# Kernel optimization log

Measured on AMD Instinct MI355X. Metric: run time of the kernel, lower is better.

The kernel has to match this reference:

```python
import jax, jax.numpy as jnp
import numpy as np

N = 50000
E = 800000
IN_C, HID_C, OUT_C = 512, 256, 64
K = 10
ALPHA = 0.1


def setup_inputs() -> dict:
    key = jax.random.key(0)
    k1, k2, k3, k4, k5, k6 = jax.random.split(key, 6)
    x = jax.random.normal(k1, (N, IN_C), dtype=jnp.float32)
    edge_index = jax.random.randint(k2, (2, E), 0, N, dtype=jnp.int64)
    # Linear params (torch nn.Linear: y = x @ W.T + b), kaiming-ish scale
    W1 = jax.random.normal(k3, (HID_C, IN_C), dtype=jnp.float32) / np.sqrt(IN_C)
    b1 = jax.random.normal(k4, (HID_C,), dtype=jnp.float32) * 0.01
    W2 = jax.random.normal(k5, (OUT_C, HID_C), dtype=jnp.float32) / np.sqrt(HID_C)
    b2 = jax.random.normal(k6, (OUT_C,), dtype=jnp.float32) * 0.01
    return {"x": x, "edge_index": edge_index, "W1": W1, "b1": b1, "W2": W2, "b2": b2}


def reference(x, edge_index, W1, b1, W2, b2):
    # MLP head (dropout is identity in eval mode)
    h = jax.nn.relu(x @ W1.T + b1)          # [N, HID_C]
    z = h @ W2.T + b2                        # [N, OUT_C]

    src = edge_index[0]                      # message source
    dst = edge_index[1]                      # message target (aggregation index)

    # GCN symmetric normalization with self-loops (PyG APPNP default)
    ones = jnp.ones((E,), dtype=z.dtype)
    deg = jax.ops.segment_sum(ones, dst, num_segments=N) + 1.0  # +1 for self-loop
    dinv = jax.lax.rsqrt(deg)                # deg^{-1/2}
    edge_norm = (dinv[src] * dinv[dst])[:, None]   # [E, 1]
    self_norm = (dinv * dinv)[:, None]             # [N, 1] self-loop weight

    def step(hcur, _):
        agg = jax.ops.segment_sum(hcur[src] * edge_norm, dst, num_segments=N)
        agg = agg + hcur * self_norm
        hnew = (1.0 - ALPHA) * agg + ALPHA * z
        return hnew, None

    h_final, _ = jax.lax.scan(step, z, None, length=K)
    return h_final
```

## Files before the change

kernel.cpp:

```cpp
#include <hip/hip_runtime.h>

typedef __bf16 bf16x8 __attribute__((ext_vector_type(8)));
typedef float f32x4 __attribute__((ext_vector_type(4)));
typedef short short8 __attribute__((ext_vector_type(8)));

__device__ __forceinline__ unsigned short f2bf_u(float f) {
    unsigned u = __builtin_bit_cast(unsigned, f);
    u += 0x7FFFu + ((u >> 16) & 1u);
    return (unsigned short)(u >> 16);
}
__device__ __forceinline__ float bf2f(unsigned short h) {
    unsigned u = ((unsigned)h) << 16;
    return __builtin_bit_cast(float, u);
}
__device__ __forceinline__ float i2f(int b) { return __builtin_bit_cast(float, b); }

#define GLOAD_LDS16(gsrc, ldst)                                                        \
    __builtin_amdgcn_global_load_lds((const __attribute__((address_space(1))) void*)(gsrc), \
                                     (__attribute__((address_space(3))) void*)(ldst), 16, 0, 0)

__global__ __launch_bounds__(256)
void prep_a(const void* __restrict__ ei, const float* __restrict__ W1,
            const float* __restrict__ W2, int* __restrict__ flag,
            short* __restrict__ W1h, short* __restrict__ W1l,
            short* __restrict__ W2h, short* __restrict__ W2l) {
    const int tid = threadIdx.x;
    const int gtid = blockIdx.x * 256 + tid;
    const int gsize = gridDim.x * 256;
    if (blockIdx.x == 0) {
        unsigned v = 0;
        for (int i = tid * 2 + 1; i < 2048; i += 512) v |= ((const unsigned*)ei)[i];
        if (v) atomicOr(flag, 1);
    }
    const int n1 = 256 * 512, n2 = 64 * 256;
    for (int i = gtid; i < n1; i += gsize) {
        float w0 = W1[i];
        unsigned short h = f2bf_u(w0);
        W1h[i] = (short)h;
        W1l[i] = (short)f2bf_u(w0 - bf2f(h));
    }
    for (int i = gtid; i < n2; i += gsize) {
        float w0 = W2[i];
        unsigned short h = f2bf_u(w0);
        W2h[i] = (short)h;
        W2l[i] = (short)f2bf_u(w0 - bf2f(h));
    }
}

__global__ void convert_count_kernel(const void* __restrict__ edges, const int* __restrict__ flag,
                                     int* __restrict__ src, int* __restrict__ dst,
                                     int* __restrict__ counts, int E) {
    int e = blockIdx.x * 256 + threadIdx.x;
    if (e >= E) return;
    int s, d;
    if (*flag) { const int* p = (const int*)edges; s = p[e]; d = p[E + e]; }
    else       { const long long* p = (const long long*)edges; s = (int)p[e]; d = (int)p[E + e]; }
    src[e] = s;
    dst[e] = d;
    atomicAdd(&counts[d], 1);
}

__global__ void bsum_dinv_kernel(const int* __restrict__ counts, float* __restrict__ dinv,
                                 int* __restrict__ bs, int n) {
    __shared__ int sdata[256];
    int i = blockIdx.x * 256 + threadIdx.x;
    int v = (i < n) ? counts[i] : 0;
    if (i < n) dinv[i] = rsqrtf((float)v + 1.0f);
    sdata[threadIdx.x] = v;
    __syncthreads();
    #pragma unroll
    for (int off = 128; off > 0; off >>= 1) {
        if (threadIdx.x < off) sdata[threadIdx.x] += sdata[threadIdx.x + off];
        __syncthreads();
    }
    if (threadIdx.x == 0) bs[blockIdx.x] = sdata[0];
}

__global__ void scanbs_kernel(const int* __restrict__ bs, int* __restrict__ bsoff, int nb) {
    __shared__ int sdata[256];
    int tid = threadIdx.x;
    int v = (tid < nb) ? bs[tid] : 0;
    sdata[tid] = v;
    __syncthreads();
    #pragma unroll
    for (int off = 1; off < 256; off <<= 1) {
        int t = (tid >= off) ? sdata[tid - off] : 0;
        __syncthreads();
        sdata[tid] += t;
        __syncthreads();
    }
    if (tid < nb) bsoff[tid] = sdata[tid] - v;
}

__global__ void scanblock_kernel(const int* __restrict__ counts, const int* __restrict__ bsoff,
                                 int* __restrict__ rowptr, int* __restrict__ cursor, int n) {
    __shared__ int sdata[256];
    int tid = threadIdx.x;
    int i = blockIdx.x * 256 + tid;
    int v = (i < n) ? counts[i] : 0;
    sdata[tid] = v;
    __syncthreads();
    #pragma unroll
    for (int off = 1; off < 256; off <<= 1) {
        int t = (tid >= off) ? sdata[tid - off] : 0;
        __syncthreads();
        sdata[tid] += t;
        __syncthreads();
    }
    int excl = bsoff[blockIdx.x] + sdata[tid] - v;
    if (i < n) { rowptr[i] = excl; cursor[i] = excl; }
    if (i == n - 1) rowptr[n] = excl + v;
}

__global__ void fill_kernel(const int* __restrict__ src, const int* __restrict__ dst,
                            const float* __restrict__ dinv, int* __restrict__ cursor,
                            int2* __restrict__ csr, int E) {
    int e = blockIdx.x * 256 + threadIdx.x;
    if (e >= E) return;
    int s = src[e], d = dst[e];
    int pos = atomicAdd(&cursor[d], 1);
    float w = dinv[s] * dinv[d];
    csr[pos] = make_int2(s, __builtin_bit_cast(int, w));
}

__global__ __launch_bounds__(512)
void gemm1f_k(const float* __restrict__ x, const short* __restrict__ Bh,
              const short* __restrict__ Bl, const float* __restrict__ bias,
              short* __restrict__ C, int M) {
    extern __shared__ short lds[];
    short* sA  = lds;
    short* sBh = lds + 16384;
    short* sBl = lds + 49152;
    const int KDIM = 512, LDC = 256;
    const int tid = threadIdx.x, lane = tid & 63, wave = tid >> 6;
    const int wr = wave >> 2, wc = wave & 3;
    const int m0 = blockIdx.x * 128;
    const int lr = lane & 15, lk = lane >> 4;
    const int l8r = lane >> 3, l8u = lane & 7;
    const int tr = tid >> 3, tk = tid & 7;

    f32x4 acc[4][4];
    #pragma unroll
    for (int mi = 0; mi < 4; ++mi)
        #pragma unroll
        for (int ni = 0; ni < 4; ++ni) acc[mi][ni] = {0.f, 0.f, 0.f, 0.f};

    float4 fa[2][2];

    auto a_load = [&](int k0) {
        #pragma unroll
        for (int p = 0; p < 2; ++p) {
            int row = p * 64 + tr;
            int grow = m0 + row; if (grow > M - 1) grow = M - 1;
            const float* s = x + (size_t)grow * KDIM + k0 + tk * 8;
            fa[p][0] = *reinterpret_cast<const float4*>(s);
            fa[p][1] = *reinterpret_cast<const float4*>(s + 4);
        }
    };
    auto a_write = [&](int buf) {
        #pragma unroll
        for (int p = 0; p < 2; ++p) {
            int row = p * 64 + tr;
            short8 sh;
            sh[0] = (short)f2bf_u(fa[p][0].x); sh[1] = (short)f2bf_u(fa[p][0].y);
            sh[2] = (short)f2bf_u(fa[p][0].z); sh[3] = (short)f2bf_u(fa[p][0].w);
            sh[4] = (short)f2bf_u(fa[p][1].x); sh[5] = (short)f2bf_u(fa[p][1].y);
            sh[6] = (short)f2bf_u(fa[p][1].z); sh[7] = (short)f2bf_u(fa[p][1].w);
            *reinterpret_cast<short8*>(&sA[buf * 8192 + row * 64 + ((tk ^ (row & 7)) << 3)]) = sh;
        }
    };
    auto b_dma = [&](int buf, int k0) {
        #pragma unroll
        for (int p = 0; p < 4; ++p) {
            int row = p * 64 + wave * 8 + l8r;
            size_t goff = (size_t)row * KDIM + k0 + ((l8u ^ (row & 7)) << 3);
            GLOAD_LDS16(Bh + goff, sBh + buf * 16384 + (p * 64 + wave * 8) * 64);
            GLOAD_LDS16(Bl + goff, sBl + buf * 16384 + (p * 64 + wave * 8) * 64);
        }
    };

    a_load(0);
    b_dma(0, 0);
    asm volatile("s_waitcnt vmcnt(0)" ::: "memory");
    a_write(0);
    __syncthreads();

    int cur = 0;
    #pragma unroll 1
    for (int t = 0; t < 8; ++t) {
        const bool pf = (t < 7);
        if (pf) {
            a_load((t + 1) * 64);
            b_dma(cur ^ 1, (t + 1) * 64);
        }
        #pragma unroll
        for (int ks = 0; ks < 2; ++ks) {
            int kg = ks * 4 + lk;
            bf16x8 af[4], bhf[4], blf[4];
            #pragma unroll
            for (int mi = 0; mi < 4; ++mi) {
                int row = wr * 64 + mi * 16 + lr;
                af[mi] = *reinterpret_cast<const bf16x8*>(
                    &sA[cur * 8192 + row * 64 + ((kg ^ (row & 7)) << 3)]);
            }
            #pragma unroll
            for (int ni = 0; ni < 4; ++ni) {
                int row = wc * 64 + ni * 16 + lr;
                int idx = cur * 16384 + row * 64 + ((kg ^ (row & 7)) << 3);
                bhf[ni] = *reinterpret_cast<const bf16x8*>(&sBh[idx]);
                blf[ni] = *reinterpret_cast<const bf16x8*>(&sBl[idx]);
            }
            #pragma unroll
            for (int mi = 0; mi < 4; ++mi)
                #pragma unroll
                for (int ni = 0; ni < 4; ++ni) {
                    acc[mi][ni] = __builtin_amdgcn_mfma_f32_16x16x32_bf16(af[mi], bhf[ni], acc[mi][ni], 0, 0, 0);
                    acc[mi][ni] = __builtin_amdgcn_mfma_f32_16x16x32_bf16(af[mi], blf[ni], acc[mi][ni], 0, 0, 0);
                }
        }
        asm volatile("s_waitcnt vmcnt(0)" ::: "memory");
        if (pf) a_write(cur ^ 1);
        __syncthreads();
        cur ^= 1;
    }

    #pragma unroll
    for (int ni = 0; ni < 4; ++ni) {
        int col = wc * 64 + ni * 16 + lr;
        float bv = bias[col];
        #pragma unroll
        for (int mi = 0; mi < 4; ++mi) {
            #pragma unroll
            for (int r = 0; r < 4; ++r) {
                int row = m0 + wr * 64 + mi * 16 + lk * 4 + r;
                if (row < M) {
                    float v = fmaxf(acc[mi][ni][r] + bv, 0.0f);
                    C[(size_t)row * LDC + col] = (short)f2bf_u(v);
                }
            }
        }
    }
}

template<int KDIM, int LDC, bool AF32, bool RELU>
__device__ __forceinline__
void gemm_tile(const void* __restrict__ Av, const short* __restrict__ Bh,
               const short* __restrict__ Bl, const float* __restrict__ bias,
               short* __restrict__ C, int M, int m0, int n0,
               short* sAp, short* sBp) {
    constexpr int NT = KDIM / 64;
    const int tid  = threadIdx.x;
    const int lane = tid & 63;
    const int wave = tid >> 6;
    const int wr = wave >> 1, wc = wave & 1;
    const int lr = lane & 15;
    const int lk = lane >> 4;
    const int l8r = lane >> 3;
    const int l8u = lane & 7;
    const int tr = tid >> 3;
    const int tk = tid & 7;

    f32x4 acc[2][2];
    #pragma unroll
    for (int mi = 0; mi < 2; ++mi)
        #pragma unroll
        for (int ni = 0; ni < 2; ++ni) acc[mi][ni] = {0.f, 0.f, 0.f, 0.f};

    float4 fa[2][2];

    auto a_load = [&](int k0) {
        #pragma unroll
        for (int p = 0; p < 2; ++p) {
            int row = p * 64 + tr;
            int grow = m0 + row; if (grow > M - 1) grow = M - 1;
            const float* s = (const float*)Av + (size_t)grow * KDIM + k0 + tk * 8;
            fa[p][0] = *reinterpret_cast<const float4*>(s);
            fa[p][1] = *reinterpret_cast<const float4*>(s + 4);
        }
    };
    auto a_write = [&](int buf) {
        #pragma unroll
        for (int p = 0; p < 2; ++p) {
            int row = p * 64 + tr;
            short8 sh;
            sh[0] = (short)f2bf_u(fa[p][0].x); sh[1] = (short)f2bf_u(fa[p][0].y);
            sh[2] = (short)f2bf_u(fa[p][0].z); sh[3] = (short)f2bf_u(fa[p][0].w);
            sh[4] = (short)f2bf_u(fa[p][1].x); sh[5] = (short)f2bf_u(fa[p][1].y);
            sh[6] = (short)f2bf_u(fa[p][1].z); sh[7] = (short)f2bf_u(fa[p][1].w);
            *reinterpret_cast<short8*>(&sAp[buf * 8192 + row * 64 + ((tk ^ (row & 7)) << 3)]) = sh;
        }
    };
    auto a_dma = [&](int buf, int k0) {
        #pragma unroll
        for (int p = 0; p < 2; ++p) {
            int row = p * 64 + wave * 8 + l8r;
            int grow = m0 + row; if (grow > M - 1) grow = M - 1;
            const short* s = (const short*)Av + (size_t)grow * KDIM + k0 + ((l8u ^ (row & 7)) << 3);
            GLOAD_LDS16(s, sAp + buf * 8192 + p * 4096 + wave * 512);
        }
    };
    auto b_dma = [&](int buf, int k0) {
        int row = wave * 8 + l8r;
        size_t goff = (size_t)(n0 + row) * KDIM + k0 + ((l8u ^ (row & 7)) << 3);
        GLOAD_LDS16(Bh + goff, sBp + (buf * 2 + 0) * 4096 + wave * 512);
        GLOAD_LDS16(Bl + goff, sBp + (buf * 2 + 1) * 4096 + wave * 512);
    };

    if (AF32) {
        a_load(0);
        b_dma(0, 0);
        asm volatile("s_waitcnt vmcnt(0)" ::: "memory");
        a_write(0);
        __syncthreads();
    } else {
        a_dma(0, 0);
        b_dma(0, 0);
        asm volatile("s_waitcnt vmcnt(0)" ::: "memory");
        __builtin_amdgcn_s_barrier();
        asm volatile("" ::: "memory");
    }

    int cur = 0;
    #pragma unroll 1
    for (int t = 0; t < NT; ++t) {
        const bool pf = (t + 1 < NT);
        if (pf) {
            if (AF32) a_load((t + 1) * 64);
            else      a_dma(cur ^ 1, (t + 1) * 64);
            b_dma(cur ^ 1, (t + 1) * 64);
        }
        #pragma unroll
        for (int ks = 0; ks < 2; ++ks) {
            int kg = ks * 4 + lk;
            bf16x8 af[2], bhf[2], blf[2];
            #pragma unroll
            for (int mi = 0; mi < 2; ++mi) {
                int row = wr * 32 + mi * 16 + lr;
                af[mi] = *reinterpret_cast<const bf16x8*>(
                    &sAp[cur * 8192 + row * 64 + ((kg ^ (row & 7)) << 3)]);
            }
            #pragma unroll
            for (int ni = 0; ni < 2; ++ni) {
                int row = wc * 32 + ni * 16 + lr;
                int idx = row * 64 + ((kg ^ (row & 7)) << 3);
                bhf[ni] = *reinterpret_cast<const bf16x8*>(&sBp[(cur * 2 + 0) * 4096 + idx]);
                blf[ni] = *reinterpret_cast<const bf16x8*>(&sBp[(cur * 2 + 1) * 4096 + idx]);
            }
            #pragma unroll
            for (int mi = 0; mi < 2; ++mi)
                #pragma unroll
                for (int ni = 0; ni < 2; ++ni) {
                    acc[mi][ni] = __builtin_amdgcn_mfma_f32_16x16x32_bf16(af[mi], bhf[ni], acc[mi][ni], 0, 0, 0);
                    acc[mi][ni] = __builtin_amdgcn_mfma_f32_16x16x32_bf16(af[mi], blf[ni], acc[mi][ni], 0, 0, 0);
                }
        }
        asm volatile("s_waitcnt vmcnt(0)" ::: "memory");
        if (AF32) { if (pf) a_write(cur ^ 1); __syncthreads(); }
        else { __builtin_amdgcn_s_barrier(); asm volatile("" ::: "memory"); }
        cur ^= 1;
    }

    #pragma unroll
    for (int ni = 0; ni < 2; ++ni) {
        int col = n0 + wc * 32 + ni * 16 + lr;
        float bv = bias[col];
        #pragma unroll
        for (int mi = 0; mi < 2; ++mi) {
            #pragma unroll
            for (int r = 0; r < 4; ++r) {
                int row = m0 + wr * 32 + mi * 16 + lk * 4 + r;
                if (row < M) {
                    float v = acc[mi][ni][r] + bv;
                    if (RELU) v = fmaxf(v, 0.0f);
                    C[(size_t)row * LDC + col] = (short)f2bf_u(v);
                }
            }
        }
    }
}

__global__ __launch_bounds__(512)
void gemm1_k(const float* __restrict__ x, const short* __restrict__ W1h,
             const short* __restrict__ W1l, const float* __restrict__ b1,
             short* __restrict__ Hbf, int M) {
    __shared__ short sAp[2 * 128 * 64];
    __shared__ short sBp[2 * 2 * 64 * 64];
    int t = blockIdx.x;
    gemm_tile<512, 256, true, true>(x, W1h, W1l, b1, Hbf, M, (t >> 2) * 128, (t & 3) * 64, sAp, sBp);
}

__global__ __launch_bounds__(512)
void gemm2_k(const short* __restrict__ Hbf, const short* __restrict__ W2h,
             const short* __restrict__ W2l, const float* __restrict__ b2,
             short* __restrict__ zbf, int M) {
    __shared__ short sAp[2 * 128 * 64];
    __shared__ short sBp[2 * 2 * 64 * 64];
    gemm_tile<256, 64, false, false>(Hbf, W2h, W2l, b2, zbf, M, blockIdx.x * 128, 0, sAp, sBp);
}

__global__ __launch_bounds__(256)
void prop_step(const unsigned short* __restrict__ hin, const unsigned short* __restrict__ zbf,
               const int* __restrict__ rowptr, const int2* __restrict__ csr,
               const float* __restrict__ dinv, void* __restrict__ hout,
               int outf32, int n) {
    int node = blockIdx.x * 4 + (threadIdx.x >> 6);
    int lane = threadIdx.x & 63;
    if (node >= n) return;
    float di = dinv[node];
    int base = node << 6;
    float acc = bf2f(hin[base + lane]) * (di * di);
    int e = rowptr[node], e1 = rowptr[node + 1];

    if (e + 8 <= e1) {
        int2 r[8];
        #pragma unroll
        for (int j = 0; j < 8; ++j) r[j] = csr[e + j];
        for (; e + 16 <= e1; e += 8) {
            int2 rn[8];
            #pragma unroll
            for (int j = 0; j < 8; ++j) rn[j] = csr[e + 8 + j];
            unsigned short v[8];
            #pragma unroll
            for (int j = 0; j < 8; ++j) v[j] = hin[((unsigned)r[j].x << 6) + lane];
            #pragma unroll
            for (int j = 0; j < 8; ++j) acc = fmaf(bf2f(v[j]), i2f(r[j].y), acc);
            #pragma unroll
            for (int j = 0; j < 8; ++j) r[j] = rn[j];
        }
        {
            unsigned short v[8];
            #pragma unroll
            for (int j = 0; j < 8; ++j) v[j] = hin[((unsigned)r[j].x << 6) + lane];
            #pragma unroll
            for (int j = 0; j < 8; ++j) acc = fmaf(bf2f(v[j]), i2f(r[j].y), acc);
            e += 8;
        }
    }
    for (; e + 4 <= e1; e += 4) {
        int2 r[4]; unsigned short v[4];
        #pragma unroll
        for (int j = 0; j < 4; ++j) r[j] = csr[e + j];
        #pragma unroll
        for (int j = 0; j < 4; ++j) v[j] = hin[((unsigned)r[j].x << 6) + lane];
        #pragma unroll
        for (int j = 0; j < 4; ++j) acc = fmaf(bf2f(v[j]), i2f(r[j].y), acc);
    }
    for (; e < e1; ++e) {
        int2 r = csr[e];
        acc = fmaf(bf2f(hin[((unsigned)r.x << 6) + lane]), i2f(r.y), acc);
    }

    float res = 0.9f * acc + 0.1f * bf2f(zbf[base + lane]);
    if (outf32) ((float*)hout)[base + lane] = res;
    else        ((unsigned short*)hout)[base + lane] = f2bf_u(res);
}

extern "C" void kernel_launch(void* const* d_in, const int* in_sizes, int n_in,
                              void* d_out, int out_size, void* d_ws, size_t ws_size,
                              hipStream_t stream) {
    const float* x  = (const float*)d_in[0];
    const void*  ei = d_in[1];
    const float* W1 = (const float*)d_in[2];
    const float* b1 = (const float*)d_in[3];
    const float* W2 = (const float*)d_in[4];
    const float* b2 = (const float*)d_in[5];
    float* dout = (float*)d_out;

    const int IN_C = 512, HID_C = 256, OUT_C = 64, Ksteps = 10;
    const int N = in_sizes[0] / IN_C;
    const int E = in_sizes[1] / 2;

    char* w = (char*)d_ws;
    auto alloc = [&](size_t bytes) { char* p = w; w += (bytes + 255) & ~(size_t)255; return p; };
    int*   flag    = (int*)  alloc(4);
    int*   src32   = (int*)  alloc((size_t)E * 4);
    int*   dst32   = (int*)  alloc((size_t)E * 4);
    int*   counts  = (int*)  alloc((size_t)N * 4);
    int*   rowptr  = (int*)  alloc((size_t)(N + 1) * 4);
    int*   cursor  = (int*)  alloc((size_t)N * 4);
    float* dinv    = (float*)alloc((size_t)N * 4);
    int2*  csr     = (int2*) alloc((size_t)E * 8);
    short* W1h     = (short*)alloc((size_t)HID_C * IN_C * 2);
    short* W1l     = (short*)alloc((size_t)HID_C * IN_C * 2);
    short* W2h     = (short*)alloc((size_t)OUT_C * HID_C * 2);
    short* W2l     = (short*)alloc((size_t)OUT_C * HID_C * 2);
    short* Hbf     = (short*)alloc((size_t)N * HID_C * 2);
    unsigned short* zbf = (unsigned short*)alloc((size_t)N * OUT_C * 2);
    unsigned short* hA  = (unsigned short*)alloc((size_t)N * OUT_C * 2);
    unsigned short* hB  = (unsigned short*)alloc((size_t)N * OUT_C * 2);
    int*   bs      = (int*)  alloc(256 * 4);
    int*   bsoff   = (int*)  alloc(256 * 4);

    hipMemsetAsync(flag, 0, 4, stream);
    hipMemsetAsync(counts, 0, (size_t)N * 4, stream);

    const int egrid = (E + 255) / 256;
    const int nblk = (N + 255) / 256;
    const int mgrid = (N + 127) / 128;
    const int pgrid = (N + 3) / 4;

    prep_a<<<512, 256, 0, stream>>>(ei, W1, W2, flag, W1h, W1l, W2h, W2l);
    convert_count_kernel<<<egrid, 256, 0, stream>>>(ei, flag, src32, dst32, counts, E);
    bsum_dinv_kernel<<<nblk, 256, 0, stream>>>(counts, dinv, bs, N);
    scanbs_kernel<<<1, 256, 0, stream>>>(bs, bsoff, nblk);
    scanblock_kernel<<<nblk, 256, 0, stream>>>(counts, bsoff, rowptr, cursor, N);
    fill_kernel<<<egrid, 256, 0, stream>>>(src32, dst32, dinv, cursor, csr, E);

    constexpr int G1_LDS = 163840;
    bool big = hipFuncSetAttribute((const void*)gemm1f_k,
                                   hipFuncAttributeMaxDynamicSharedMemorySize,
                                   G1_LDS) == hipSuccess;
    if (big) {
        gemm1f_k<<<mgrid, 512, G1_LDS, stream>>>(x, W1h, W1l, b1, Hbf, N);
        if (hipGetLastError() != hipSuccess) big = false;
    }
    if (!big) {
        gemm1_k<<<mgrid * 4, 512, 0, stream>>>(x, W1h, W1l, b1, Hbf, N);
    }
    gemm2_k<<<mgrid, 512, 0, stream>>>(Hbf, W2h, W2l, b2, (short*)zbf, N);

    const unsigned short* pin = zbf;
    for (int s = 0; s < Ksteps; ++s) {
        bool last = (s == Ksteps - 1);
        void* out = last ? (void*)dout : ((s & 1) ? (void*)hB : (void*)hA);
        prop_step<<<pgrid, 256, 0, stream>>>(pin, zbf, rowptr, csr, dinv,
                                             out, last ? 1 : 0, N);
        pin = (const unsigned short*)out;
    }
}
```

Before: 452.1 us.

## Fold self-loops into CSR and retile GEMM1 to 256-row, K=32 stages

Self-loop edges are now written into the CSR during the scan, so the propagation kernel handles them as ordinary edges instead of doing a separate dinv load and multiply-add per node. Separately, the first GEMM now processes 256 rows per block with a 32-wide K slice (16 stages instead of 8) and a smaller LDS footprint. The larger M tile reuses the W1 tiles more, and the smaller LDS may let more blocks fit per CU. The cost is more loop iterations with more barriers, more accumulator registers per thread, and an extra edge per node in each propagation step.

```diff
diff --git a/kernel.cpp b/kernel.cpp
--- a/kernel.cpp
+++ b/kernel.cpp
@@ -66,7 +66,7 @@
     int i = blockIdx.x * 256 + threadIdx.x;
     int v = (i < n) ? counts[i] : 0;
     if (i < n) dinv[i] = rsqrtf((float)v + 1.0f);
-    sdata[threadIdx.x] = v;
+    sdata[threadIdx.x] = (i < n) ? (v + 1) : 0;
     __syncthreads();
     #pragma unroll
     for (int off = 128; off > 0; off >>= 1) {
@@ -93,11 +93,13 @@
 }
 
 __global__ void scanblock_kernel(const int* __restrict__ counts, const int* __restrict__ bsoff,
-                                 int* __restrict__ rowptr, int* __restrict__ cursor, int n) {
+                                 const float* __restrict__ dinv,
+                                 int* __restrict__ rowptr, int* __restrict__ cursor,
+                                 int2* __restrict__ csr, int n) {
     __shared__ int sdata[256];
     int tid = threadIdx.x;
     int i = blockIdx.x * 256 + tid;
-    int v = (i < n) ? counts[i] : 0;
+    int v = (i < n) ? (counts[i] + 1) : 0;
     sdata[tid] = v;
     __syncthreads();
     #pragma unroll
@@ -108,7 +110,12 @@
         __syncthreads();
     }
     int excl = bsoff[blockIdx.x] + sdata[tid] - v;
-    if (i < n) { rowptr[i] = excl; cursor[i] = excl; }
+    if (i < n) {
+        rowptr[i] = excl;
+        float di = dinv[i];
+        csr[excl] = make_int2(i, __builtin_bit_cast(int, di * di));
+        cursor[i] = excl + 1;
+    }
     if (i == n - 1) rowptr[n] = excl + v;
 }
 
@@ -130,52 +137,53 @@
     extern __shared__ short lds[];
     short* sA  = lds;
     short* sBh = lds + 16384;
-    short* sBl = lds + 49152;
+    short* sBl = lds + 32768;
     const int KDIM = 512, LDC = 256;
     const int tid = threadIdx.x, lane = tid & 63, wave = tid >> 6;
     const int wr = wave >> 2, wc = wave & 3;
-    const int m0 = blockIdx.x * 128;
+    const int m0 = blockIdx.x * 256;
     const int lr = lane & 15, lk = lane >> 4;
-    const int l8r = lane >> 3, l8u = lane & 7;
-    const int tr = tid >> 3, tk = tid & 7;
-
-    f32x4 acc[4][4];
-    #pragma unroll
-    for (int mi = 0; mi < 4; ++mi)
+    const int l4r = lane >> 2, l4u = lane & 3;
+    const int arow = tid >> 1, ahalf = tid & 1;
+
+    f32x4 acc[8][4];
+    #pragma unroll
+    for (int mi = 0; mi < 8; ++mi)
         #pragma unroll
         for (int ni = 0; ni < 4; ++ni) acc[mi][ni] = {0.f, 0.f, 0.f, 0.f};
 
-    float4 fa[2][2];
+    float4 fa[4];
 
     auto a_load = [&](int k0) {
+        int grow = m0 + arow; if (grow > M - 1) grow = M - 1;
+        const float* s = x + (size_t)grow * KDIM + k0 + ahalf * 16;
+        fa[0] = ((const float4*)s)[0];
+        fa[1] = ((const float4*)s)[1];
+        fa[2] = ((const float4*)s)[2];
+        fa[3] = ((const float4*)s)[3];
+    };
+    auto a_write = [&](int buf) {
+        short8 s0, s1;
+        s0[0] = (short)f2bf_u(fa[0].x); s0[1] = (short)f2bf_u(fa[0].y);
+        s0[2] = (short)f2bf_u(fa[0].z); s0[3] = (short)f2bf_u(fa[0].w);
+        s0[4] = (short)f2bf_u(fa[1].x); s0[5] = (short)f2bf_u(fa[1].y);
+        s0[6] = (short)f2bf_u(fa[1].z); s0[7] = (short)f2bf_u(fa[1].w);
+        s1[0] = (short)f2bf_u(fa[2].x); s1[1] = (short)f2bf_u(fa[2].y);
+        s1[2] = (short)f2bf_u(fa[2].z); s1[3] = (short)f2bf_u(fa[2].w);
+        s1[4] = (short)f2bf_u(fa[3].x); s1[5] = (short)f2bf_u(fa[3].y);
+        s1[6] = (short)f2bf_u(fa[3].z); s1[7] = (short)f2bf_u(fa[3].w);
+        int b = buf * 8192 + arow * 32;
+        *reinterpret_cast<short8*>(&sA[b + (((2 * ahalf)     ^ (arow & 3)) << 3)]) = s0;
+        *reinterpret_cast<short8*>(&sA[b + (((2 * ahalf + 1) ^ (arow & 3)) << 3)]) = s1;
+    };
+    auto b_dma = [&](int buf, int k0) {
         #pragma unroll
         for (int p = 0; p < 2; ++p) {
-            int row = p * 64 + tr;
-            int grow = m0 + row; if (grow > M - 1) grow = M - 1;
-            const float* s = x + (size_t)grow * KDIM + k0 + tk * 8;
-            fa[p][0] = *reinterpret_cast<const float4*>(s);
-            fa[p][1] = *reinterpret_cast<const float4*>(s + 4);
-        }
-    };
-    auto a_write = [&](int buf) {
-        #pragma unroll
-        for (int p = 0; p < 2; ++p) {
-            int row = p * 64 + tr;
-            short8 sh;
-            sh[0] = (short)f2bf_u(fa[p][0].x); sh[1] = (short)f2bf_u(fa[p][0].y);
-            sh[2] = (short)f2bf_u(fa[p][0].z); sh[3] = (short)f2bf_u(fa[p][0].w);
-            sh[4] = (short)f2bf_u(fa[p][1].x); sh[5] = (short)f2bf_u(fa[p][1].y);
-            sh[6] = (short)f2bf_u(fa[p][1].z); sh[7] = (short)f2bf_u(fa[p][1].w);
-            *reinterpret_cast<short8*>(&sA[buf * 8192 + row * 64 + ((tk ^ (row & 7)) << 3)]) = sh;
-        }
-    };
-    auto b_dma = [&](int buf, int k0) {
-        #pragma unroll
-        for (int p = 0; p < 4; ++p) {
-            int row = p * 64 + wave * 8 + l8r;
-            size_t goff = (size_t)row * KDIM + k0 + ((l8u ^ (row & 7)) << 3);
-            GLOAD_LDS16(Bh + goff, sBh + buf * 16384 + (p * 64 + wave * 8) * 64);
-            GLOAD_LDS16(Bl + goff, sBl + buf * 16384 + (p * 64 + wave * 8) * 64);
+            int row = p * 128 + wave * 16 + l4r;
+            size_t goff = (size_t)row * KDIM + k0 + ((l4u ^ (row & 3)) << 3);
+            int db = buf * 8192 + (p * 128 + wave * 16) * 32;
+            GLOAD_LDS16(Bh + goff, sBh + db);
+            GLOAD_LDS16(Bl + goff, sBl + db);
         }
     };
 
@@ -187,31 +195,29 @@
 
     int cur = 0;
     #pragma unroll 1
-    for (int t = 0; t < 8; ++t) {
-        const bool pf = (t < 7);
+    for (int t = 0; t < 16; ++t) {
+        const bool pf = (t < 15);
         if (pf) {
-            a_load((t + 1) * 64);
-            b_dma(cur ^ 1, (t + 1) * 64);
-        }
-        #pragma unroll
-        for (int ks = 0; ks < 2; ++ks) {
-            int kg = ks * 4 + lk;
-            bf16x8 af[4], bhf[4], blf[4];
-            #pragma unroll
-            for (int mi = 0; mi < 4; ++mi) {
-                int row = wr * 64 + mi * 16 + lr;
+            a_load((t + 1) * 32);
+            b_dma(cur ^ 1, (t + 1) * 32);
+        }
+        {
+            bf16x8 af[8], bhf[4], blf[4];
+            #pragma unroll
+            for (int mi = 0; mi < 8; ++mi) {
+                int row = wr * 128 + mi * 16 + lr;
                 af[mi] = *reinterpret_cast<const bf16x8*>(
-                    &sA[cur * 8192 + row * 64 + ((kg ^ (row & 7)) << 3)]);
+                    &sA[cur * 8192 + row * 32 + ((lk ^ (row & 3)) << 3)]);
             }
             #pragma unroll
             for (int ni = 0; ni < 4; ++ni) {
                 int row = wc * 64 + ni * 16 + lr;
-                int idx = cur * 16384 + row * 64 + ((kg ^ (row & 7)) << 3);
+                int idx = cur * 8192 + row * 32 + ((lk ^ (row & 3)) << 3);
                 bhf[ni] = *reinterpret_cast<const bf16x8*>(&sBh[idx]);
                 blf[ni] = *reinterpret_cast<const bf16x8*>(&sBl[idx]);
             }
             #pragma unroll
-            for (int mi = 0; mi < 4; ++mi)
+            for (int mi = 0; mi < 8; ++mi)
                 #pragma unroll
                 for (int ni = 0; ni < 4; ++ni) {
                     acc[mi][ni] = __builtin_amdgcn_mfma_f32_16x16x32_bf16(af[mi], bhf[ni], acc[mi][ni], 0, 0, 0);
@@ -229,10 +235,10 @@
         int col = wc * 64 + ni * 16 + lr;
         float bv = bias[col];
         #pragma unroll
-        for (int mi = 0; mi < 4; ++mi) {
+        for (int mi = 0; mi < 8; ++mi) {
             #pragma unroll
             for (int r = 0; r < 4; ++r) {
-                int row = m0 + wr * 64 + mi * 16 + lk * 4 + r;
+                int row = m0 + wr * 128 + mi * 16 + lk * 4 + r;
                 if (row < M) {
                     float v = fmaxf(acc[mi][ni][r] + bv, 0.0f);
                     C[(size_t)row * LDC + col] = (short)f2bf_u(v);
@@ -401,14 +407,12 @@
 __global__ __launch_bounds__(256)
 void prop_step(const unsigned short* __restrict__ hin, const unsigned short* __restrict__ zbf,
                const int* __restrict__ rowptr, const int2* __restrict__ csr,
-               const float* __restrict__ dinv, void* __restrict__ hout,
-               int outf32, int n) {
+               void* __restrict__ hout, int outf32, int n) {
     int node = blockIdx.x * 4 + (threadIdx.x >> 6);
+    if (node >= n) return;
     int lane = threadIdx.x & 63;
-    if (node >= n) return;
-    float di = dinv[node];
     int base = node << 6;
-    float acc = bf2f(hin[base + lane]) * (di * di);
+    float acc = 0.0f;
     int e = rowptr[node], e1 = rowptr[node + 1];
 
     if (e + 8 <= e1) {
@@ -479,7 +483,7 @@
     int*   rowptr  = (int*)  alloc((size_t)(N + 1) * 4);
     int*   cursor  = (int*)  alloc((size_t)N * 4);
     float* dinv    = (float*)alloc((size_t)N * 4);
-    int2*  csr     = (int2*) alloc((size_t)E * 8);
+    int2*  csr     = (int2*) alloc((size_t)(E + N) * 8);
     short* W1h     = (short*)alloc((size_t)HID_C * IN_C * 2);
     short* W1l     = (short*)alloc((size_t)HID_C * IN_C * 2);
     short* W2h     = (short*)alloc((size_t)OUT_C * HID_C * 2);
@@ -496,34 +500,34 @@
 
     const int egrid = (E + 255) / 256;
     const int nblk = (N + 255) / 256;
-    const int mgrid = (N + 127) / 128;
     const int pgrid = (N + 3) / 4;
 
     prep_a<<<512, 256, 0, stream>>>(ei, W1, W2, flag, W1h, W1l, W2h, W2l);
     convert_count_kernel<<<egrid, 256, 0, stream>>>(ei, flag, src32, dst32, counts, E);
     bsum_dinv_kernel<<<nblk, 256, 0, stream>>>(counts, dinv, bs, N);
     scanbs_kernel<<<1, 256, 0, stream>>>(bs, bsoff, nblk);
-    scanblock_kernel<<<nblk, 256, 0, stream>>>(counts, bsoff, rowptr, cursor, N);
+    scanblock_kernel<<<nblk, 256, 0, stream>>>(counts, bsoff, dinv, rowptr, cursor, csr, N);
     fill_kernel<<<egrid, 256, 0, stream>>>(src32, dst32, dinv, cursor, csr, E);
 
-    constexpr int G1_LDS = 163840;
+    constexpr int G1_LDS = 98304;
+    const int g1grid = (N + 255) / 256;
     bool big = hipFuncSetAttribute((const void*)gemm1f_k,
                                    hipFuncAttributeMaxDynamicSharedMemorySize,
                                    G1_LDS) == hipSuccess;
     if (big) {
-        gemm1f_k<<<mgrid, 512, G1_LDS, stream>>>(x, W1h, W1l, b1, Hbf, N);
+        gemm1f_k<<<g1grid, 512, G1_LDS, stream>>>(x, W1h, W1l, b1, Hbf, N);
         if (hipGetLastError() != hipSuccess) big = false;
     }
     if (!big) {
-        gemm1_k<<<mgrid * 4, 512, 0, stream>>>(x, W1h, W1l, b1, Hbf, N);
-    }
-    gemm2_k<<<mgrid, 512, 0, stream>>>(Hbf, W2h, W2l, b2, (short*)zbf, N);
+        gemm1_k<<<((N + 127) / 128) * 4, 512, 0, stream>>>(x, W1h, W1l, b1, Hbf, N);
+    }
+    gemm2_k<<<(N + 127) / 128, 512, 0, stream>>>(Hbf, W2h, W2l, b2, (short*)zbf, N);
 
     const unsigned short* pin = zbf;
     for (int s = 0; s < Ksteps; ++s) {
         bool last = (s == Ksteps - 1);
         void* out = last ? (void*)dout : ((s & 1) ? (void*)hB : (void*)hA);
-        prop_step<<<pgrid, 256, 0, stream>>>(pin, zbf, rowptr, csr, dinv,
+        prop_step<<<pgrid, 256, 0, stream>>>(pin, zbf, rowptr, csr,
                                              out, last ? 1 : 0, N);
         pin = (const unsigned short*)out;
     }
```

Measured after the change: 453.4 us. About the same (+0.3%).
